# Kernel tuning notes

Hardware: AMD Instinct MI355X
Metric: run time of the kernel (lower is better)

The kernel has to match this reference:

```python
import jax, jax.numpy as jnp
import numpy as np
from itertools import combinations

SEQ_LEN = 10; WAY = 5; SHOT = 5; TSS = 2
IN_DIM = 2048; OUT_DIM = 2048
PAIRS = np.array(list(combinations(range(SEQ_LEN), TSS)))  # [T, 2] frame-pair indices
T = PAIRS.shape[0]  # 45 tuples


def _cdist(a, b):
    # Euclidean distance matrix, stable form: sqrt(|a|^2 + |b|^2 - 2 a.b)
    a2 = jnp.sum(a * a, axis=-1)[:, None]
    b2 = jnp.sum(b * b, axis=-1)[None, :]
    sq = a2 + b2 - 2.0 * (a @ b.T)
    return jnp.sqrt(jnp.maximum(sq, 0.0))


def setup_inputs() -> dict:
    key = jax.random.key(0)
    k1, k2, k3, k4 = jax.random.split(key, 4)
    n_s = WAY * SHOT            # 25
    n_q = WAY * 15              # 75
    support_set = jax.random.normal(k1, (n_s, SEQ_LEN, IN_DIM), jnp.float32)
    queries = jax.random.normal(k2, (n_q, SEQ_LEN, IN_DIM), jnp.float32)
    # class-sorted labels: class c occupies rows [c*SHOT, (c+1)*SHOT)
    support_labels = jnp.arange(n_s, dtype=jnp.int32) // SHOT
    lim = 1.0 / np.sqrt(IN_DIM * TSS)
    clsW_w = jax.random.uniform(k3, (OUT_DIM, IN_DIM * TSS), jnp.float32, -lim, lim)
    clsW_b = jax.random.uniform(k4, (OUT_DIM,), jnp.float32, -lim, lim)
    return {"support_set": support_set, "support_labels": support_labels,
            "queries": queries, "clsW_w": clsW_w, "clsW_b": clsW_b}


def _forward(support_set, queries, clsW_w, clsW_b):
    n_s, n_q = support_set.shape[0], queries.shape[0]
    D2 = TSS * IN_DIM
    # tuple gather: [n, T, 2*in_dim] (dropout is eval-mode identity)
    sup = support_set[:, PAIRS, :].reshape(n_s, T, D2)
    qry = queries[:, PAIRS, :].reshape(n_q, T, D2)
    q_embed = jax.nn.relu(qry.reshape(n_q * T, D2) @ clsW_w.T + clsW_b)      # [nqT, D]
    sup_c = sup.reshape(WAY, SHOT * T, D2)                                    # labels sorted by class
    support_all = jax.nn.relu(jnp.einsum('csd,od->cso', sup_c, clsW_w) + clsW_b)  # [way, sT, D]

    distmat = jax.vmap(lambda s: _cdist(q_embed, s))(support_all)             # [way, nqT, sT]
    # torch: view(-1, T, shot).topk(k=1, dim=1).mean -> max over reshaped axis
    dist_class = distmat.reshape(WAY, n_q * T, T, SHOT).max(axis=2)           # [way, nqT, shot]
    ave_dist_all = dist_class.mean(axis=2)                                    # [way, nqT]
    dist_min = distmat.min(axis=2).reshape(WAY, n_q, T).mean(axis=2).T        # [n_q, way] (computed, unused downstream)
    dist_max = distmat.max(axis=2).reshape(WAY, n_q, T).mean(axis=2).T        # [n_q, way]
    pos_all = jnp.argmax(distmat, axis=2)                                     # [way, nqT]

    cols = []
    for c in range(WAY):
        mse = support_all[c][pos_all[c]]                                      # [nqT, D]
        other = support_all[np.array([m for m in range(WAY) if m != c])]      # [way-1, sT, D]
        other_flat = other.reshape((WAY - 1) * SHOT * T, OUT_DIM)
        cosd = _cdist(mse, other_flat).reshape(n_q * T, WAY - 1, SHOT * T)
        cosd = cosd.transpose(1, 0, 2)                                        # [way-1, nqT, sT]
        # record_pos[idx, s2] = #{s1 : cosd[idx,s1,s2] > ave_dist_all[c, s1]}
        record = jnp.sum(cosd > ave_dist_all[c][None, :, None], axis=1).astype(jnp.float32)  # [way-1, sT]
        nz = jnp.maximum(jnp.sum(record != 0, axis=1), 1).astype(jnp.float32)
        thr = record.sum(axis=1) / nz                                         # mean over nonzero entries
        mask = (record < thr[:, None]).astype(jnp.float32)                    # selected columns per other-class
        # diff_embed = concat of selected rows; mean of cdist over them == masked mean
        d_full = _cdist(q_embed, other_flat)                                  # [nqT, (way-1)*sT]
        msum = jnp.maximum(mask.sum(), 1.0)
        mean_d = (d_full * mask.reshape(-1)[None, :]).sum(axis=1) / msum      # [nqT]
        cols.append(mean_d.reshape(n_q, T).mean(axis=1) / (WAY - 1))
    dist_contrast = jnp.stack(cols, axis=1)                                   # [n_q, way]

    logits_contrast = dist_max / (dist_contrast + dist_max)
    return dist_max, logits_contrast


def reference(support_set, support_labels, queries, clsW_w, clsW_b):
    # support_labels are sorted class blocks (arange // shot); class gather is a reshape
    return _forward(support_set, queries, clsW_w, clsW_b)
```

## Files before the change

kernel.cpp:

```cpp
#include <hip/hip_runtime.h>


typedef __bf16 bf16x8 __attribute__((ext_vector_type(8)));
typedef float f32x4 __attribute__((ext_vector_type(4)));

#define NQT   3375
#define MROWS 4500
#define MPAD  4608
#define LDD   1152
#define BK    32

__constant__ int P0[45] = {0,0,0,0,0,0,0,0,0,
                           1,1,1,1,1,1,1,1,
                           2,2,2,2,2,2,2,
                           3,3,3,3,3,3,
                           4,4,4,4,4,
                           5,5,5,5,
                           6,6,6,
                           7,7,
                           8};
__constant__ int P1[45] = {1,2,3,4,5,6,7,8,9,
                           2,3,4,5,6,7,8,9,
                           3,4,5,6,7,8,9,
                           4,5,6,7,8,9,
                           5,6,7,8,9,
                           6,7,8,9,
                           7,8,9,
                           8,9,
                           9};

__device__ inline unsigned short f2b(float x) {
  __bf16 b = (__bf16)x;
  return __builtin_bit_cast(unsigned short, b);
}
__device__ inline float b2f(unsigned int u16) {
  return __uint_as_float(u16 << 16);
}

__device__ __forceinline__ void gl_lds16(const unsigned short* g, unsigned short* l) {
  __builtin_amdgcn_global_load_lds(
      (__attribute__((address_space(1))) void*)(g),
      (__attribute__((address_space(3))) void*)(l),
      16, 0, 0);
}

__global__ void prep(const float* __restrict__ W, const float* __restrict__ Q,
                     const float* __restrict__ Sp,
                     unsigned short* __restrict__ Ws, unsigned short* __restrict__ X,
                     float* __restrict__ record, float* __restrict__ sq) {
  int b = blockIdx.x, tid = threadIdx.x;
  if (b < 8192) {
    int i = b * 256 + tid;
    int i4 = i << 2;
    int o  = i4 >> 12;
    int k  = i4 & 4095;
    int hf = k >> 11;
    int kk = k & 2047;
    float4 v = reinterpret_cast<const float4*>(W)[i];
    ushort4 u;
    u.x = f2b(v.x); u.y = f2b(v.y); u.z = f2b(v.z); u.w = f2b(v.w);
    *reinterpret_cast<ushort4*>(Ws + (size_t)(o + hf * 2048) * 2048 + kk) = u;
  } else if (b < 10240) {
    int i = (b - 8192) * 256 + tid;
    ushort4 u = {0, 0, 0, 0};
    if (i < 384000) {
      float4 v = reinterpret_cast<const float4*>(Q)[i];
      u.x = f2b(v.x); u.y = f2b(v.y); u.z = f2b(v.z); u.w = f2b(v.w);
    } else if (i < 512000) {
      float4 v = reinterpret_cast<const float4*>(Sp)[i - 384000];
      u.x = f2b(v.x); u.y = f2b(v.y); u.z = f2b(v.z); u.w = f2b(v.w);
    }
    reinterpret_cast<ushort4*>(X)[i] = u;
  } else {
    int i = (b - 10240) * 256 + tid;
    if (i < 4500) record[i] = 0.f;
    else if (i < 4500 + 4608) sq[i - 4500] = 0.f;
  }
}

__global__ __launch_bounds__(512)
void gemm_ring(const unsigned short* __restrict__ A, const unsigned short* __restrict__ B,
               int lda, int ldb, int Ksplit,
               float* __restrict__ Pout0, float* __restrict__ Pout1, int ldd) {
  __shared__ unsigned short As[3][128 * BK];
  __shared__ unsigned short Bs[3][128 * BK];
  const int tid  = threadIdx.x;
  const int wave = tid >> 6, lane = tid & 63;
  const int quad = lane >> 4, l16 = lane & 15;
  const int wm = (wave >> 2) * 64, wn = (wave & 3) * 32;
  const int m0 = blockIdx.x * 128, n0 = blockIdx.y * 128;
  const int kbase = blockIdx.z * Ksplit;

  f32x4 acc[4][2];
#pragma unroll
  for (int i = 0; i < 4; ++i)
#pragma unroll
    for (int j = 0; j < 2; ++j) {
      f32x4 z = {0.f, 0.f, 0.f, 0.f};
      acc[i][j] = z;
    }

  const int r0  = tid >> 2;
  const int qsw = (tid & 3) ^ ((tid >> 3) & 3);
  const int kp0 = qsw * 8;
  const int rsw = (quad ^ ((l16 >> 1) & 3)) * 8;
  const unsigned short* pa = A + (size_t)(m0 + r0) * lda + kbase + kp0;
  const unsigned short* pb = B + (size_t)(n0 + r0) * ldb + kbase + kp0;
  const int NKi = Ksplit / BK;

#define ISSUE(kk, st) do {                                 \
    gl_lds16(pa + (size_t)(kk) * BK, &As[st][wave * 512]); \
    gl_lds16(pb + (size_t)(kk) * BK, &Bs[st][wave * 512]); \
  } while (0)

  ISSUE(0, 0);
  ISSUE(1, 1);
  asm volatile("s_waitcnt vmcnt(2)" ::: "memory");
  __builtin_amdgcn_s_barrier();

  int sc = 0;
  for (int k = 0; k < NKi; ++k) {
    int sn = sc + 2; if (sn >= 3) sn -= 3;
    if (k + 2 < NKi) ISSUE(k + 2, sn);
    bf16x8 af[4], bfr[2];
#pragma unroll
    for (int t = 0; t < 4; ++t)
      af[t] = *reinterpret_cast<const bf16x8*>(&As[sc][(wm + t * 16 + l16) * BK + rsw]);
#pragma unroll
    for (int t = 0; t < 2; ++t)
      bfr[t] = *reinterpret_cast<const bf16x8*>(&Bs[sc][(wn + t * 16 + l16) * BK + rsw]);
#pragma unroll
    for (int i = 0; i < 4; ++i)
#pragma unroll
      for (int j = 0; j < 2; ++j)
        acc[i][j] = __builtin_amdgcn_mfma_f32_16x16x32_bf16(af[i], bfr[j], acc[i][j], 0, 0, 0);
    if (k + 1 < NKi) {
      if (k + 2 < NKi) asm volatile("s_waitcnt vmcnt(2)" ::: "memory");
      else             asm volatile("s_waitcnt vmcnt(0)" ::: "memory");
      __builtin_amdgcn_s_barrier();
    }
    sc = sc + 1; if (sc >= 3) sc = 0;
  }
#undef ISSUE
  asm volatile("s_waitcnt vmcnt(0)" ::: "memory");

  float* Pout = blockIdx.z ? Pout1 : Pout0;
#pragma unroll
  for (int i = 0; i < 4; ++i)
#pragma unroll
    for (int j = 0; j < 2; ++j) {
      int col = n0 + wn + j * 16 + l16;
      int rbase = m0 + wm + i * 16 + quad * 4;
      f32x4 v = acc[i][j];
#pragma unroll
      for (int r = 0; r < 4; ++r)
        Pout[(size_t)(rbase + r) * ldd + col] = v[r];
    }
}

__global__ __launch_bounds__(256)
void build_e2(const float* __restrict__ Y0, const float* __restrict__ Y1,
              const float* __restrict__ bias,
              unsigned short* __restrict__ E, float* __restrict__ sq) {
  int b = blockIdx.x, tid = threadIdx.x;
  if (b >= 400) {
    const size_t base = (size_t)4500 * 2048 / 8;
    const int total = 108 * 2048 / 8;
    uint4 z = {0, 0, 0, 0};
    for (int i = (b - 400) * 256 + tid; i < total; i += 512)
      reinterpret_cast<uint4*>(E)[base + i] = z;
    return;
  }
  int n = b >> 2, q = b & 3;
  int c0 = q * 512;
  __shared__ float Lf[10][512];
  __shared__ float Rf[10][512];
  for (int e = tid; e < 1280; e += 256) {
    int f  = e >> 7;
    int cc = (e & 127) << 2;
    const float* ya = Y0 + (size_t)(n * 10 + f) * 4096;
    const float* yb = Y1 + (size_t)(n * 10 + f) * 4096;
    float4 l0 = *reinterpret_cast<const float4*>(ya + c0 + cc);
    float4 l1 = *reinterpret_cast<const float4*>(yb + c0 + cc);
    float4 r0 = *reinterpret_cast<const float4*>(ya + 2048 + c0 + cc);
    float4 r1 = *reinterpret_cast<const float4*>(yb + 2048 + c0 + cc);
    float4 L = {l0.x + l1.x, l0.y + l1.y, l0.z + l1.z, l0.w + l1.w};
    float4 R = {r0.x + r1.x, r0.y + r1.y, r0.z + r1.z, r0.w + r1.w};
    *reinterpret_cast<float4*>(&Lf[f][cc]) = L;
    *reinterpret_cast<float4*>(&Rf[f][cc]) = R;
  }
  __syncthreads();
  int wv = tid >> 6, lane = tid & 63;
  int erow0 = (n < 75) ? n * 45 : NQT + (n - 75) * 45;
  for (int t = wv; t < 45; t += 4) {
    int f0 = P0[t], f1 = P1[t];
    int row = erow0 + t;
    float s = 0.f;
#pragma unroll
    for (int k = 0; k < 8; ++k) {
      int c = lane + 64 * k;
      float x = Lf[f0][c] + Rf[f1][c] + bias[c0 + c];
      x = fmaxf(x, 0.f);
      unsigned short ob = f2b(x);
      E[(size_t)row * 2048 + c0 + c] = ob;
      float xr = b2f(ob);
      s += xr * xr;
    }
#pragma unroll
    for (int sh = 32; sh > 0; sh >>= 1) s += __shfl_down(s, sh, 64);
    if (lane == 0) atomicAdd(&sq[row], s);
  }
}

__global__ __launch_bounds__(320)
void dist_stats(const float* __restrict__ Pa, const float* __restrict__ Pb,
                const float* __restrict__ sq, float* __restrict__ D,
                float* __restrict__ ave, int* __restrict__ pos,
                float* __restrict__ rmax) {
  __shared__ float drow[LDD];
  __shared__ float sm[5][64];
  int row = blockIdx.x, tid = threadIdx.x;
  float sr = sq[row];
  if (tid < 288) {
    int c = tid * 4;
    size_t ix = (size_t)row * LDD / 4 + tid;
    float4 a = reinterpret_cast<const float4*>(Pa)[ix];
    float4 bb = reinterpret_cast<const float4*>(Pb)[ix];
    float4 o;
    o.x = sqrtf(fmaxf(sr + sq[NQT + c + 0] - 2.f * (a.x + bb.x), 0.f));
    o.y = sqrtf(fmaxf(sr + sq[NQT + c + 1] - 2.f * (a.y + bb.y), 0.f));
    o.z = sqrtf(fmaxf(sr + sq[NQT + c + 2] - 2.f * (a.z + bb.z), 0.f));
    o.w = sqrtf(fmaxf(sr + sq[NQT + c + 3] - 2.f * (a.w + bb.w), 0.f));
    reinterpret_cast<float4*>(D)[ix] = o;
    *reinterpret_cast<float4*>(&drow[c]) = o;
  }
  __syncthreads();
  if (row >= NQT) return;
  int wv = tid >> 6, lane = tid & 63;
  const float* p = &drow[wv * 225];
  float best = -1e30f; int bi = 225;
  float gm = -1e30f;
  if (lane < 60) {
#pragma unroll
    for (int r = 0; r < 4; ++r) {
      int j = lane + 60 * r;
      if (j < 225) {
        float v = p[j];
        if (v > best) { best = v; bi = j; }
        gm = fmaxf(gm, v);
      }
    }
  }
#pragma unroll
  for (int s = 32; s > 0; s >>= 1) {
    float vv = __shfl_down(best, s, 64);
    int   ii = __shfl_down(bi,   s, 64);
    if (vv > best || (vv == best && ii < bi)) { best = vv; bi = ii; }
  }
  sm[wv][lane] = gm;
  __builtin_amdgcn_wave_barrier();
  if (lane < 5) {
    float m = -1e30f;
#pragma unroll
    for (int a = 0; a < 12; ++a) m = fmaxf(m, sm[wv][lane + 5 * a]);
    sm[wv][lane] = m;
  }
  __builtin_amdgcn_wave_barrier();
  if (lane == 0) {
    float s5 = sm[wv][0] + sm[wv][1] + sm[wv][2] + sm[wv][3] + sm[wv][4];
    ave[wv * NQT + row]  = s5 * 0.2f;
    pos[wv * NQT + row]  = bi;
    rmax[wv * NQT + row] = best;
  }
}

__global__ void record_part(const float* __restrict__ D, const float* __restrict__ ave,
                            const int* __restrict__ pos, float* __restrict__ record) {
  int b = blockIdx.x;
  int c = b / 135, chunk = b - c * 135;
  int i0 = chunk * 25;
  int tid = threadIdx.x;
  __shared__ int   sp[25];
  __shared__ float sa[25];
  if (tid < 25) {
    sp[tid] = pos[c * NQT + i0 + tid];
    sa[tid] = ave[c * NQT + i0 + tid];
  }
  __syncthreads();
  float cnt[4] = {0.f, 0.f, 0.f, 0.f};
  int gcol[4];
#pragma unroll
  for (int j = 0; j < 4; ++j) {
    int col = tid + j * 256;
    gcol[j] = (col < 900) ? (col < c * 225 ? col : col + 225) : 0;
  }
  const bool act3 = (tid + 768) < 900;
  const float* Dsup = D + (size_t)(NQT + c * 225) * LDD;
  for (int ii = 0; ii < 25; ++ii) {
    const float* row = Dsup + (size_t)sp[ii] * LDD;
    float a = sa[ii];
    cnt[0] += (row[gcol[0]] > a) ? 1.f : 0.f;
    cnt[1] += (row[gcol[1]] > a) ? 1.f : 0.f;
    cnt[2] += (row[gcol[2]] > a) ? 1.f : 0.f;
    if (act3) cnt[3] += (row[gcol[3]] > a) ? 1.f : 0.f;
  }
#pragma unroll
  for (int j = 0; j < 4; ++j) {
    int col = tid + j * 256;
    if (col < 900) atomicAdd(&record[c * 900 + col], cnt[j]);
  }
}

__global__ __launch_bounds__(256)
void tail_fused(const float* __restrict__ D, const float* __restrict__ record,
                const float* __restrict__ rmax, float* __restrict__ out) {
  int q = blockIdx.x;
  int tid = threadIdx.x;
  int wv = tid >> 6, lane = tid & 63;
  __shared__ float maskT[5 * LDD];
  __shared__ float msum_s[5];
  __shared__ float St[5][45];
  for (int i = tid; i < 5 * LDD; i += 256) maskT[i] = 0.f;
  if (tid < 5) msum_s[tid] = 0.f;
  __syncthreads();

  for (int seg = wv; seg < 20; seg += 4) {
    int c = seg >> 2, mi = seg & 3;
    const float* rec = record + c * 900 + mi * 225;
    float r0 = rec[lane];
    float r1 = rec[lane + 64];
    float r2 = rec[lane + 128];
    float r3 = (lane + 192 < 225) ? rec[lane + 192] : 0.f;
    float s  = r0 + r1 + r2 + r3;
    float nz = (r0 != 0.f ? 1.f : 0.f) + (r1 != 0.f ? 1.f : 0.f) +
               (r2 != 0.f ? 1.f : 0.f) + (r3 != 0.f ? 1.f : 0.f);
#pragma unroll
    for (int sh = 32; sh > 0; sh >>= 1) {
      s  += __shfl_down(s,  sh, 64);
      nz += __shfl_down(nz, sh, 64);
    }
    s  = __shfl(s,  0, 64);
    nz = __shfl(nz, 0, 64);
    float nzc = nz < 1.f ? 1.f : nz;
    float thr = s / nzc;
    float mcount = 0.f;
    float rv[4] = {r0, r1, r2, r3};
#pragma unroll
    for (int j = 0; j < 4; ++j) {
      int idx = lane + j * 64;
      if (idx < 225) {
        float m = (rv[j] < thr) ? 1.f : 0.f;
        int L = mi * 225 + idx;
        int g = L + (L >= c * 225 ? 225 : 0);
        maskT[c * LDD + g] = m;
        mcount += m;
      }
    }
#pragma unroll
    for (int sh = 32; sh > 0; sh >>= 1) mcount += __shfl_down(mcount, sh, 64);
    if (lane == 0) atomicAdd(&msum_s[c], mcount);
  }
  __syncthreads();

  for (int t = wv; t < 45; t += 4) {
    const float* row = D + (size_t)(q * 45 + t) * LDD;
    float a0 = 0.f, a1 = 0.f, a2 = 0.f, a3 = 0.f, a4 = 0.f;
#pragma unroll
    for (int k = 0; k < 18; ++k) {
      int col = k * 64 + lane;
      float d = row[col];
      a0 += d * maskT[0 * LDD + col];
      a1 += d * maskT[1 * LDD + col];
      a2 += d * maskT[2 * LDD + col];
      a3 += d * maskT[3 * LDD + col];
      a4 += d * maskT[4 * LDD + col];
    }
#pragma unroll
    for (int sh = 32; sh > 0; sh >>= 1) {
      a0 += __shfl_down(a0, sh, 64);
      a1 += __shfl_down(a1, sh, 64);
      a2 += __shfl_down(a2, sh, 64);
      a3 += __shfl_down(a3, sh, 64);
      a4 += __shfl_down(a4, sh, 64);
    }
    if (lane == 0) {
      St[0][t] = a0; St[1][t] = a1; St[2][t] = a2; St[3][t] = a3; St[4][t] = a4;
    }
  }
  __syncthreads();

  if (tid < 5) {
    int c = tid;
    float dsum = 0.f, ssum = 0.f;
    for (int t = 0; t < 45; ++t) {
      dsum += rmax[c * NQT + q * 45 + t];
      ssum += St[c][t];
    }
    float dm = dsum / 45.f;
    float ms = msum_s[c]; if (ms < 1.f) ms = 1.f;
    float contrast = ssum / (ms * 180.f);
    out[q * 5 + c] = dm;
    out[375 + q * 5 + c] = dm / (contrast + dm);
  }
}

extern "C" void kernel_launch(void* const* d_in, const int* in_sizes, int n_in,
                              void* d_out, int out_size, void* d_ws, size_t ws_size,
                              hipStream_t stream) {
  const float* support = (const float*)d_in[0];
  const float* queries = (const float*)d_in[2];
  const float* W       = (const float*)d_in[3];
  const float* bias    = (const float*)d_in[4];
  float* out = (float*)d_out;

  char* ws = (char*)d_ws;
  size_t off = 0;
  unsigned short* Xb  = (unsigned short*)(ws + off);
  unsigned short* Wsp = (unsigned short*)(ws + off + 4194304);
  float*          Pd1 = (float*)(ws + off);          off += 21233664;
  float*          Y0  = (float*)(ws + off);          off += (size_t)1024 * 4096 * 4;
  float*          Dm  = (float*)(ws + off);
  float*          Y1  = (float*)(ws + off);          off += (size_t)MPAD * LDD * 4;
  unsigned short* Eb  = (unsigned short*)(ws + off); off += (size_t)MPAD * 2048 * 2;
  float* sq      = (float*)(ws + off); off += 4608 * 4 + 256;
  float* ave     = (float*)(ws + off); off += 5 * NQT * 4 + 256;
  int*   pos     = (int*)(ws + off);   off += 5 * NQT * 4 + 256;
  float* rmax    = (float*)(ws + off); off += 5 * NQT * 4 + 256;
  float* record  = (float*)(ws + off); off += 5 * 900 * 4 + 256;

  prep<<<10276, 256, 0, stream>>>(W, queries, support, Wsp, Xb, record, sq);

  dim3 g1(1024 / 128, 4096 / 128, 2);
  gemm_ring<<<g1, 512, 0, stream>>>(Xb, Wsp, 2048, 2048, 1024, Y0, Y1, 4096);

  build_e2<<<402, 256, 0, stream>>>(Y0, Y1, bias, Eb, sq);

  dim3 g2(MPAD / 128, LDD / 128, 2);
  gemm_ring<<<g2, 512, 0, stream>>>(Eb, Eb + (size_t)NQT * 2048, 2048, 2048, 1024,
                                    Dm, Pd1, LDD);

  dist_stats<<<MROWS, 320, 0, stream>>>(Dm, Pd1, sq, Dm, ave, pos, rmax);

  record_part<<<675, 256, 0, stream>>>(Dm, ave, pos, record);
  tail_fused<<<75, 256, 0, stream>>>(Dm, record, rmax, out);
}
```

Measured before the change: 213.9 us.

## Fuse split-K reduction and distance epilogue into GEMM via last-block counter

```diff
diff --git a/kernel.cpp b/kernel.cpp
--- a/kernel.cpp
+++ b/kernel.cpp
@@ -47,7 +47,8 @@
 __global__ void prep(const float* __restrict__ W, const float* __restrict__ Q,
                      const float* __restrict__ Sp,
                      unsigned short* __restrict__ Ws, unsigned short* __restrict__ X,
-                     float* __restrict__ record, float* __restrict__ sq) {
+                     float* __restrict__ record, float* __restrict__ sq,
+                     int* __restrict__ cnt) {
   int b = blockIdx.x, tid = threadIdx.x;
   if (b < 8192) {
     int i = b * 256 + tid;
@@ -74,14 +75,16 @@
   } else {
     int i = (b - 10240) * 256 + tid;
     if (i < 4500) record[i] = 0.f;
-    else if (i < 4500 + 4608) sq[i - 4500] = 0.f;
+    else if (i < 9108) sq[i - 4500] = 0.f;
+    else if (i < 9432) cnt[i - 9108] = 0;
   }
 }
 
 __global__ __launch_bounds__(512)
 void gemm_ring(const unsigned short* __restrict__ A, const unsigned short* __restrict__ B,
                int lda, int ldb, int Ksplit,
-               float* __restrict__ Pout0, float* __restrict__ Pout1, int ldd) {
+               float* Pout0, float* Pout1, int ldd,
+               const float* __restrict__ sqv, float* Dfin, int* cnt) {
   __shared__ unsigned short As[3][128 * BK];
   __shared__ unsigned short Bs[3][128 * BK];
   const int tid  = threadIdx.x;
@@ -156,6 +159,35 @@
       for (int r = 0; r < 4; ++r)
         Pout[(size_t)(rbase + r) * ldd + col] = v[r];
     }
+
+  if (Dfin == nullptr) return;
+  __threadfence();
+  __shared__ int lastf;
+  if (tid == 0)
+    lastf = (atomicAdd(&cnt[blockIdx.y * gridDim.x + blockIdx.x], 1) == 1);
+  __syncthreads();
+  if (!lastf) return;
+  __threadfence();
+  const float* Po = blockIdx.z ? Pout0 : Pout1;
+#pragma unroll
+  for (int i = 0; i < 4; ++i) {
+    int rbase = m0 + wm + i * 16 + quad * 4;
+    float sr[4];
+#pragma unroll
+    for (int r = 0; r < 4; ++r) sr[r] = sqv[rbase + r];
+#pragma unroll
+    for (int j = 0; j < 2; ++j) {
+      int col = n0 + wn + j * 16 + l16;
+      float scq = sqv[NQT + col];
+      f32x4 v = acc[i][j];
+#pragma unroll
+      for (int r = 0; r < 4; ++r) {
+        float p = v[r] + Po[(size_t)(rbase + r) * ldd + col];
+        Dfin[(size_t)(rbase + r) * ldd + col] =
+            sqrtf(fmaxf(sr[r] + scq - 2.f * p, 0.f));
+      }
+    }
+  }
 }
 
 __global__ __launch_bounds__(256)
@@ -213,29 +245,16 @@
 }
 
 __global__ __launch_bounds__(320)
-void dist_stats(const float* __restrict__ Pa, const float* __restrict__ Pb,
-                const float* __restrict__ sq, float* __restrict__ D,
-                float* __restrict__ ave, int* __restrict__ pos,
-                float* __restrict__ rmax) {
+void stats_only(const float* __restrict__ D, float* __restrict__ ave,
+                int* __restrict__ pos, float* __restrict__ rmax) {
   __shared__ float drow[LDD];
   __shared__ float sm[5][64];
   int row = blockIdx.x, tid = threadIdx.x;
-  float sr = sq[row];
   if (tid < 288) {
-    int c = tid * 4;
     size_t ix = (size_t)row * LDD / 4 + tid;
-    float4 a = reinterpret_cast<const float4*>(Pa)[ix];
-    float4 bb = reinterpret_cast<const float4*>(Pb)[ix];
-    float4 o;
-    o.x = sqrtf(fmaxf(sr + sq[NQT + c + 0] - 2.f * (a.x + bb.x), 0.f));
-    o.y = sqrtf(fmaxf(sr + sq[NQT + c + 1] - 2.f * (a.y + bb.y), 0.f));
-    o.z = sqrtf(fmaxf(sr + sq[NQT + c + 2] - 2.f * (a.z + bb.z), 0.f));
-    o.w = sqrtf(fmaxf(sr + sq[NQT + c + 3] - 2.f * (a.w + bb.w), 0.f));
-    reinterpret_cast<float4*>(D)[ix] = o;
-    *reinterpret_cast<float4*>(&drow[c]) = o;
-  }
-  __syncthreads();
-  if (row >= NQT) return;
+    reinterpret_cast<float4*>(drow)[tid] = reinterpret_cast<const float4*>(D)[ix];
+  }
+  __syncthreads();
   int wv = tid >> 6, lane = tid & 63;
   const float* p = &drow[wv * 225];
   float best = -1e30f; int bi = 225;
@@ -311,7 +330,7 @@
   }
 }
 
-__global__ __launch_bounds__(256)
+__global__ __launch_bounds__(512)
 void tail_fused(const float* __restrict__ D, const float* __restrict__ record,
                 const float* __restrict__ rmax, float* __restrict__ out) {
   int q = blockIdx.x;
@@ -320,11 +339,11 @@
   __shared__ float maskT[5 * LDD];
   __shared__ float msum_s[5];
   __shared__ float St[5][45];
-  for (int i = tid; i < 5 * LDD; i += 256) maskT[i] = 0.f;
+  for (int i = tid; i < 5 * LDD; i += 512) maskT[i] = 0.f;
   if (tid < 5) msum_s[tid] = 0.f;
   __syncthreads();
 
-  for (int seg = wv; seg < 20; seg += 4) {
+  for (int seg = wv; seg < 20; seg += 8) {
     int c = seg >> 2, mi = seg & 3;
     const float* rec = record + c * 900 + mi * 225;
     float r0 = rec[lane];
@@ -362,7 +381,7 @@
   }
   __syncthreads();
 
-  for (int t = wv; t < 45; t += 4) {
+  for (int t = wv; t < 45; t += 8) {
     const float* row = D + (size_t)(q * 45 + t) * LDD;
     float a0 = 0.f, a1 = 0.f, a2 = 0.f, a3 = 0.f, a4 = 0.f;
 #pragma unroll
@@ -427,20 +446,22 @@
   int*   pos     = (int*)(ws + off);   off += 5 * NQT * 4 + 256;
   float* rmax    = (float*)(ws + off); off += 5 * NQT * 4 + 256;
   float* record  = (float*)(ws + off); off += 5 * 900 * 4 + 256;
-
-  prep<<<10276, 256, 0, stream>>>(W, queries, support, Wsp, Xb, record, sq);
+  int*   cnt     = (int*)(ws + off);   off += 324 * 4 + 256;
+
+  prep<<<10277, 256, 0, stream>>>(W, queries, support, Wsp, Xb, record, sq, cnt);
 
   dim3 g1(1024 / 128, 4096 / 128, 2);
-  gemm_ring<<<g1, 512, 0, stream>>>(Xb, Wsp, 2048, 2048, 1024, Y0, Y1, 4096);
+  gemm_ring<<<g1, 512, 0, stream>>>(Xb, Wsp, 2048, 2048, 1024, Y0, Y1, 4096,
+                                    nullptr, nullptr, nullptr);
 
   build_e2<<<402, 256, 0, stream>>>(Y0, Y1, bias, Eb, sq);
 
   dim3 g2(MPAD / 128, LDD / 128, 2);
   gemm_ring<<<g2, 512, 0, stream>>>(Eb, Eb + (size_t)NQT * 2048, 2048, 2048, 1024,
-                                    Dm, Pd1, LDD);
-
-  dist_stats<<<MROWS, 320, 0, stream>>>(Dm, Pd1, sq, Dm, ave, pos, rmax);
+                                    Dm, Pd1, LDD, sq, Dm, cnt);
+
+  stats_only<<<NQT, 320, 0, stream>>>(Dm, ave, pos, rmax);
 
   record_part<<<675, 256, 0, stream>>>(Dm, ave, pos, record);
-  tail_fused<<<75, 256, 0, stream>>>(Dm, record, rmax, out);
-}
+  tail_fused<<<75, 512, 0, stream>>>(Dm, record, rmax, out);
+}
```

Result: slower. 466.0 us (+117.9%).
